# Kernel tuning notes

Measured on AMD Instinct MI355X. Metric: run time of the kernel, lower is better.

## Reference

```python
import jax, jax.numpy as jnp
import numpy as np
import math

EMB = 1024
HEADS = 16
VOCAB = 32000


def gelu_tanh(x):
    c = math.sqrt(2.0 / math.pi)
    return 0.5 * x * (1.0 + jnp.tanh(c * (x + 0.044715 * x * x * x)))


def layernorm(x, w, b, eps=1e-5):
    mean = jnp.mean(x, axis=-1, keepdims=True)
    var = jnp.var(x, axis=-1, keepdims=True)  # unbiased=False
    return w * ((x - mean) / jnp.sqrt(var + eps)) + b


def setup_inputs() -> dict:
    key = jax.random.key(0)
    ks = jax.random.split(key, 12)
    E, H, V = EMB, HEADS, VOCAB
    s = 1.0 / math.sqrt(E)
    return {
        "x": jax.random.normal(ks[0], (2, 2048, E), dtype=jnp.float32),
        "W_q": jax.random.normal(ks[1], (E, E), dtype=jnp.float32) * s,
        "W_k": jax.random.normal(ks[2], (E, E), dtype=jnp.float32) * s,
        "W_v": jax.random.normal(ks[3], (E, E), dtype=jnp.float32) * s,
        "ln1_w": jnp.ones((E,), jnp.float32),
        "ln1_b": jnp.zeros((E,), jnp.float32),
        "ln2_w": jnp.ones((E,), jnp.float32),
        "ln2_b": jnp.zeros((E,), jnp.float32),
        "ff_w1": jax.random.normal(ks[4], (E, 4 * E), dtype=jnp.float32) * s,
        "ff_b1": jnp.zeros((4 * E,), jnp.float32),
        "ff_w2": jax.random.normal(ks[5], (4 * E, E), dtype=jnp.float32) * (0.5 * s),
        "ff_b2": jnp.zeros((E,), jnp.float32),
        "proj_w": jax.random.normal(ks[6], (E, V), dtype=jnp.float32) * s,
        "proj_b": jnp.zeros((V,), jnp.float32),
    }


def attention(x, W_q, W_k, W_v):
    B, S, E = x.shape
    H = HEADS
    D = E // H
    q = (x @ W_q).reshape(B, S, H, D).transpose(0, 2, 1, 3)  # [B,H,S,D]
    k = (x @ W_k).reshape(B, S, H, D).transpose(0, 2, 1, 3)
    v = (x @ W_v).reshape(B, S, H, D).transpose(0, 2, 1, 3)
    scores = jnp.einsum("bhqd,bhkd->bhqk", q, k) / math.sqrt(D)
    causal = jnp.tril(jnp.ones((S, S), dtype=bool))
    scores = jnp.where(causal[None, None], scores, -jnp.inf)
    w = jax.nn.softmax(scores, axis=-1)
    ctx = jnp.einsum("bhqk,bhkd->bhqd", w, v)
    return ctx.transpose(0, 2, 1, 3).reshape(B, S, E)


def reference(x, W_q, W_k, W_v, ln1_w, ln1_b, ln2_w, ln2_b,
              ff_w1, ff_b1, ff_w2, ff_b2, proj_w, proj_b):
    # pre-LN attention block (dropout = identity, drop_rate=0)
    h = x + attention(layernorm(x, ln1_w, ln1_b), W_q, W_k, W_v)
    # pre-LN FFN block
    ff_in = layernorm(h, ln2_w, ln2_b)
    ff = gelu_tanh(ff_in @ ff_w1 + ff_b1) @ ff_w2 + ff_b2
    h = h + ff
    return h @ proj_w + proj_b
```

## Files before the change

### kernel.cpp

```cpp
#include <hip/hip_runtime.h>

using u16 = unsigned short;
typedef __attribute__((ext_vector_type(8))) short bf16x8;
typedef __attribute__((ext_vector_type(4))) float f32x4;

#define DEVI __device__ __forceinline__

DEVI float bf2f(u16 u){ union{ unsigned v; float f; } x; x.v = ((unsigned)u)<<16; return x.f; }
DEVI u16 f2bf(float f){ union{ float f; unsigned v; } x; x.f = f;
  unsigned r = x.v + 0x7FFFu + ((x.v>>16)&1u); return (u16)(r>>16); }

DEVI float gelu_f(float x){
  float y = 0.7978845608028654f*(x + 0.044715f*x*x*x);
  y = fminf(fmaxf(y, -30.f), 30.f);
  float e = __expf(2.f*y);
  return 0.5f*x*(1.f + (e-1.f)/(e+1.f));
}

DEVI void gload_lds16(const void* g, void* l){
  __builtin_amdgcn_global_load_lds((const __attribute__((address_space(1))) void*)g,
                                   (__attribute__((address_space(3))) void*)l, 16, 0, 0);
}

#define BARM asm volatile("s_barrier" ::: "memory")
#define LGKM0 asm volatile("s_waitcnt lgkmcnt(0)" ::: "memory")
#define VM8  asm volatile("s_waitcnt vmcnt(8)"  ::: "memory")
#define VM0  asm volatile("s_waitcnt vmcnt(0)"  ::: "memory")

__global__ __launch_bounds__(256) void wconv_kernel(const float* __restrict__ in,
                                                    u16* __restrict__ out, int R, int C){
  __shared__ u16 t[32][33];
  int c0 = blockIdx.x*32, r0 = blockIdx.y*32;
  int tc = threadIdx.x & 31, tr = threadIdx.x >> 5;
  #pragma unroll
  for (int i=0;i<4;i++){
    int r = tr + i*8;
    t[r][tc] = f2bf(in[(size_t)(r0+r)*C + (c0+tc)]);
  }
  __syncthreads();
  #pragma unroll
  for (int i=0;i<4;i++){
    int r = tr + i*8;
    out[(size_t)(c0+r)*R + (r0+tc)] = t[tc][r];
  }
}

DEVI void block_reduce2(float& s1, float& s2, int tid){
  #pragma unroll
  for (int off=1; off<64; off<<=1){ s1 += __shfl_xor(s1, off); s2 += __shfl_xor(s2, off); }
  __shared__ float red[8];
  int wid = tid>>6;
  if ((tid&63)==0){ red[wid*2]=s1; red[wid*2+1]=s2; }
  __syncthreads();
  s1 = red[0]+red[2]+red[4]+red[6];
  s2 = red[1]+red[3]+red[5]+red[7];
}

__global__ __launch_bounds__(256) void ln_kernel(const float* __restrict__ x,
    const float* __restrict__ w, const float* __restrict__ b, u16* __restrict__ out){
  int row = blockIdx.x, tid = threadIdx.x;
  float4 v = ((const float4*)(x + (size_t)row*1024))[tid];
  float s1 = v.x+v.y+v.z+v.w;
  float s2 = v.x*v.x+v.y*v.y+v.z*v.z+v.w*v.w;
  block_reduce2(s1,s2,tid);
  float mean = s1*(1.f/1024.f);
  float var  = s2*(1.f/1024.f) - mean*mean;
  float inv  = rsqrtf(var + 1e-5f);
  float4 wv = ((const float4*)w)[tid];
  float4 bv = ((const float4*)b)[tid];
  ushort4 o;
  o.x = f2bf(wv.x*((v.x-mean)*inv)+bv.x);
  o.y = f2bf(wv.y*((v.y-mean)*inv)+bv.y);
  o.z = f2bf(wv.z*((v.z-mean)*inv)+bv.z);
  o.w = f2bf(wv.w*((v.w-mean)*inv)+bv.w);
  ((ushort4*)(out + (size_t)row*1024))[tid] = o;
}

__global__ __launch_bounds__(256) void resln_kernel(const float* __restrict__ x,
    const u16* __restrict__ ctx, const float* __restrict__ w, const float* __restrict__ b,
    float* __restrict__ h, u16* __restrict__ hb){
  int row = blockIdx.x, tid = threadIdx.x;
  float4 xv = ((const float4*)(x + (size_t)row*1024))[tid];
  ushort4 cv = ((const ushort4*)(ctx + (size_t)row*1024))[tid];
  float4 hv;
  hv.x = xv.x + bf2f(cv.x); hv.y = xv.y + bf2f(cv.y);
  hv.z = xv.z + bf2f(cv.z); hv.w = xv.w + bf2f(cv.w);
  ((float4*)(h + (size_t)row*1024))[tid] = hv;
  float s1 = hv.x+hv.y+hv.z+hv.w;
  float s2 = hv.x*hv.x+hv.y*hv.y+hv.z*hv.z+hv.w*hv.w;
  block_reduce2(s1,s2,tid);
  float mean = s1*(1.f/1024.f);
  float var  = s2*(1.f/1024.f) - mean*mean;
  float inv  = rsqrtf(var + 1e-5f);
  float4 wv = ((const float4*)w)[tid];
  float4 bv = ((const float4*)b)[tid];
  ushort4 o;
  o.x = f2bf(wv.x*((hv.x-mean)*inv)+bv.x);
  o.y = f2bf(wv.y*((hv.y-mean)*inv)+bv.y);
  o.z = f2bf(wv.z*((hv.z-mean)*inv)+bv.z);
  o.w = f2bf(wv.w*((hv.w-mean)*inv)+bv.w);
  ((ushort4*)(hb + (size_t)row*1024))[tid] = o;
}

template<class EpiF>
DEVI void gemm8_core(const u16* __restrict__ A, const u16* __restrict__ Bt,
                     int K, int m0, int n0, EpiF epi){
  __shared__ __align__(16) u16 As[2][16384];
  __shared__ __align__(16) u16 Bs[2][16384];
  const int tid = threadIdx.x;
  const int wid = tid>>6, lane = tid&63;
  const int wr = wid>>2, wc = wid&3;
  const int g = lane>>4, l16 = lane&15;
  const int wq = wid&3;
  const int lr = lane>>3, ls = lane&7;

  f32x4 acc[8][4] = {};

  const u16* aSrc[2][2]; unsigned aDst[2][2];
  #pragma unroll
  for (int qm=0;qm<2;qm++)
    #pragma unroll
    for (int j=0;j<2;j++){
      int r = wr*128 + qm*64 + wq*16 + j*8 + lr;
      aSrc[qm][j] = A + (size_t)(m0 + r)*K + ((ls ^ (r&7))*8);
      aDst[qm][j] = (unsigned)(((wr*128 + qm*64)*8 + (wq*2+j)*64)*16);
    }
  const u16* bSrc[2][2]; unsigned bDst[2][2];
  #pragma unroll
  for (int qn=0;qn<2;qn++)
    #pragma unroll
    for (int j=0;j<2;j++){
      int r = wc*64 + qn*32 + wr*16 + j*8 + lr;
      bSrc[qn][j] = Bt + (size_t)(n0 + r)*K + ((ls ^ (r&7))*8);
      bDst[qn][j] = (unsigned)(((wc*64 + qn*32)*8 + (wr*2+j)*64)*16);
    }

  auto stageAll = [&](int buf, int kc){
    char* ab = (char*)&As[buf][0];
    char* bb = (char*)&Bs[buf][0];
    #pragma unroll
    for (int j=0;j<2;j++) gload_lds16(aSrc[0][j] + kc, ab + aDst[0][j]);
    #pragma unroll
    for (int j=0;j<2;j++) gload_lds16(bSrc[0][j] + kc, bb + bDst[0][j]);
    #pragma unroll
    for (int j=0;j<2;j++) gload_lds16(bSrc[1][j] + kc, bb + bDst[1][j]);
    #pragma unroll
    for (int j=0;j<2;j++) gload_lds16(aSrc[1][j] + kc, ab + aDst[1][j]);
  };
  auto ldA = [&](int buf, int qm, bf16x8 (&a)[4][2]){
    const char* base = (const char*)&As[buf][0];
    #pragma unroll
    for (int i=0;i<4;i++){
      int r = wr*128 + qm*64 + i*16 + l16;
      #pragma unroll
      for (int kk=0;kk<2;kk++)
        a[i][kk] = *(const bf16x8*)(base + r*128 + ((kk*64 + g*16) ^ ((l16&7)<<4)));
    }
  };
  auto ldB = [&](int buf, int qn, bf16x8 (&b)[2][2]){
    const char* base = (const char*)&Bs[buf][0];
    #pragma unroll
    for (int i=0;i<2;i++){
      int r = wc*64 + qn*32 + i*16 + l16;
      #pragma unroll
      for (int kk=0;kk<2;kk++)
        b[i][kk] = *(const bf16x8*)(base + r*128 + ((kk*64 + g*16) ^ ((l16&7)<<4)));
    }
  };
  auto mm = [&](int qm, int qn, bf16x8 (&a)[4][2], bf16x8 (&b)[2][2]){
    __builtin_amdgcn_s_setprio(1);
    #pragma unroll
    for (int i=0;i<4;i++)
      #pragma unroll
      for (int n=0;n<2;n++)
        #pragma unroll
        for (int kk=0;kk<2;kk++)
          acc[qm*4+i][qn*2+n] =
            __builtin_amdgcn_mfma_f32_16x16x32_bf16(a[i][kk], b[n][kk], acc[qm*4+i][qn*2+n], 0,0,0);
    __builtin_amdgcn_s_setprio(0);
  };

  const int NT = K>>6;
  stageAll(0, 0);
  stageAll(1, 64);

  bf16x8 a[4][2], b0[2][2], b1[2][2];
  int cur = 0;
  for (int t=0; t<NT; ++t){
    if (t < NT-1) { VM8; } else { VM0; }
    BARM;
    ldA(cur,0,a); ldB(cur,0,b0); ldB(cur,1,b1);
    mm(0,0,a,b0);
    mm(0,1,a,b1);
    ldA(cur,1,a);
    LGKM0; BARM;
    if (t+2 < NT) stageAll(cur, (t+2)<<6);
    mm(1,0,a,b0);
    mm(1,1,a,b1);
    cur ^= 1;
  }
  BARM;
  epi((char*)&As[0][0], (char*)&Bs[0][0], acc);
}

DEVI int xcd_swz(int id, int nwg){ return (id&7)*(nwg>>3) + (id>>3); }

__global__ __launch_bounds__(512,2) void proj8_kernel(const u16* __restrict__ hfb,
    const u16* __restrict__ pwt, const float* __restrict__ pb, float* __restrict__ out){
  const int xcd = blockIdx.x & 7, c = blockIdx.x >> 3;
  const int mt = 2*xcd + (c & 1);
  const int nt = c >> 1;
  const int m0 = mt*256, n0 = nt*256;
  gemm8_core(hfb, pwt, 1024, m0, n0,
    [&](char* sA, char* sB, f32x4 (&acc)[8][4]){
      const int tid = threadIdx.x;
      const int wid = tid>>6, lane = tid&63;
      const int wr = wid>>2, wc = wid&3;
      const int g = lane>>4, l16 = lane&15;
      float* ep = (float*)((wid<4 ? sA : sB) + (wid&3)*16384);
      float bb[4];
      #pragma unroll
      for (int nf=0;nf<4;nf++) bb[nf] = pb[n0 + wc*64 + nf*16 + l16];
      #pragma unroll
      for (int p=0;p<2;p++){
        #pragma unroll
        for (int mf4=0;mf4<4;mf4++){
          int mf = p*4 + mf4;
          #pragma unroll
          for (int nf=0;nf<4;nf++){
            #pragma unroll
            for (int r=0;r<4;r++)
              ep[(mf4*16 + g*4 + r)*64 + nf*16 + l16] = acc[mf][nf][r] + bb[nf];
          }
        }
        LGKM0;
        #pragma unroll
        for (int it=0;it<16;it++){
          int rl = it*4 + g;
          f32x4 v = *(const f32x4*)&ep[rl*64 + l16*4];
          int grow = m0 + wr*128 + p*64 + rl;
          __builtin_nontemporal_store(v,
            (f32x4*)&out[(size_t)grow*32000 + n0 + wc*64 + l16*4]);
        }
        LGKM0;
      }
    });
}

__global__ __launch_bounds__(512,2) void ffn1_8_kernel(const u16* __restrict__ hb,
    const u16* __restrict__ w1t, const float* __restrict__ b1, u16* __restrict__ gout){
  int swz = xcd_swz(blockIdx.x, gridDim.x);
  int mt = swz & 15, nt = swz >> 4;
  const int m0 = mt*256, n0 = nt*256;
  gemm8_core(hb, w1t, 1024, m0, n0,
    [&](char*, char*, f32x4 (&acc)[8][4]){
      const int tid = threadIdx.x;
      const int wid = tid>>6, lane = tid&63;
      const int wr = wid>>2, wc = wid&3;
      const int g = lane>>4, l16 = lane&15;
      #pragma unroll
      for (int mf=0;mf<8;mf++)
        #pragma unroll
        for (int nf=0;nf<4;nf++){
          int row = m0 + wr*128 + mf*16 + g*4;
          int col = n0 + wc*64 + nf*16 + l16;
          float bb = b1[col];
          #pragma unroll
          for (int r=0;r<4;r++)
            gout[(size_t)(row+r)*4096 + col] = f2bf(gelu_f(acc[mf][nf][r] + bb));
        }
    });
}

__global__ __launch_bounds__(512,2) void qkv8_kernel(const u16* __restrict__ xn,
    const u16* __restrict__ wqt, const u16* __restrict__ wkt, const u16* __restrict__ wvt,
    u16* __restrict__ qo, u16* __restrict__ ko, u16* __restrict__ vo){
  int swz = xcd_swz(blockIdx.x, gridDim.x);
  int mt = swz & 15, ntt = swz >> 4;
  int sel = ntt >> 2;
  const u16* Bt = (sel==0)?wqt:((sel==1)?wkt:wvt);
  u16* outp = (sel==0)?qo:((sel==1)?ko:vo);
  const int m0 = mt*256, n0 = (ntt&3)*256;
  gemm8_core(xn, Bt, 1024, m0, n0,
    [&](char*, char*, f32x4 (&acc)[8][4]){
      const int tid = threadIdx.x;
      const int wid = tid>>6, lane = tid&63;
      const int wr = wid>>2, wc = wid&3;
      const int g = lane>>4, l16 = lane&15;
      #pragma unroll
      for (int mf=0;mf<8;mf++)
        #pragma unroll
        for (int nf=0;nf<4;nf++){
          int row = m0 + wr*128 + mf*16 + g*4;
          int col = n0 + wc*64 + nf*16 + l16;
          #pragma unroll
          for (int r=0;r<4;r++)
            outp[(size_t)(row+r)*1024 + col] = f2bf(acc[mf][nf][r]);
        }
    });
}

template<int BM,int BN,int WM,int WN, class EpiF>
DEVI void gemm_core(const u16* __restrict__ A, const u16* __restrict__ Bt,
                    int K, int m0, int n0, EpiF epi){
  constexpr int WAVES_N = BN/WN;
  static_assert((BM/WM)*(BN/WN) == 4, "4 waves");
  constexpr int FM = WM/16, FN = WN/16;
  __shared__ u16 As[2][BM*32];
  __shared__ u16 Bs[2][BN*32];
  const int tid = threadIdx.x;
  const int wid = tid>>6, lane = tid&63;
  const int wr = wid / WAVES_N, wc = wid % WAVES_N;
  const int g = lane>>4, l16 = lane&15;
  f32x4 acc[FM][FN] = {};

  auto stage = [&](int buf, int t){
    #pragma unroll
    for (int j=0;j<BM/64;j++){
      int cbase = wid*BM + j*64;
      int c = cbase + lane;
      int r = c>>2, c4 = c&3;
      gload_lds16(A + (size_t)(m0+r)*K + t*32 + c4*8, &As[buf][cbase*8]);
    }
    #pragma unroll
    for (int j=0;j<BN/64;j++){
      int cbase = wid*BN + j*64;
      int c = cbase + lane;
      int r = c>>2, c4 = c&3;
      gload_lds16(Bt + (size_t)(n0+r)*K + t*32 + c4*8, &Bs[buf][cbase*8]);
    }
  };

  const int NT = K/32;
  stage(0,0);
  __syncthreads();
  for (int t=0;t<NT;t++){
    int cur = t&1;
    if (t+1 < NT) stage(cur^1, t+1);
    bf16x8 a[FM], b[FN];
    #pragma unroll
    for (int m=0;m<FM;m++) a[m] = *(const bf16x8*)&As[cur][(wr*WM + m*16 + l16)*32 + g*8];
    #pragma unroll
    for (int n=0;n<FN;n++) b[n] = *(const bf16x8*)&Bs[cur][(wc*WN + n*16 + l16)*32 + g*8];
    #pragma unroll
    for (int m=0;m<FM;m++)
      #pragma unroll
      for (int n=0;n<FN;n++)
        acc[m][n] = __builtin_amdgcn_mfma_f32_16x16x32_bf16(a[m], b[n], acc[m][n], 0,0,0);
    __syncthreads();
  }
  #pragma unroll
  for (int m=0;m<FM;m++)
    #pragma unroll
    for (int n=0;n<FN;n++){
      int row = m0 + wr*WM + m*16 + g*4;
      int col = n0 + wc*WN + n*16 + l16;
      epi(row, col, acc[m][n]);
    }
}

__global__ __launch_bounds__(256) void ffn2_kernel(const u16* __restrict__ gin,
    const u16* __restrict__ w2t, const float* __restrict__ b2,
    const float* __restrict__ h, u16* __restrict__ hfb){
  gemm_core<64,128,32,64>(gin, w2t, 4096, blockIdx.x*64, blockIdx.y*128,
    [&](int row,int col,f32x4 v){
      #pragma unroll
      for (int r=0;r<4;r++){
        float t = h[(size_t)(row+r)*1024 + col] + v[r] + b2[col];
        hfb[(size_t)(row+r)*1024 + col] = f2bf(t);
      }
    });
}

__global__ __launch_bounds__(256) void attn_kernel(const u16* __restrict__ q,
    const u16* __restrict__ k, const u16* __restrict__ v, u16* __restrict__ ctx){
  __shared__ u16 Qs[64*64], Ks[64*64], Vt[64*64];
  __shared__ u16 Ps[4][16*64];
  const int tid = threadIdx.x, lane = tid&63, wid = tid>>6;
  const int g = lane>>4, l16 = lane&15;
  const int b = blockIdx.x>>4, hh = blockIdx.x&15;
  const int qb = blockIdx.y;
  const size_t tokbase = (size_t)b*2048;
  const int hoff = hh*64;

  #pragma unroll
  for (int j=0;j<2;j++){
    int c = j*256 + tid;
    int r = c>>3, c8 = c&7;
    uint4 val = *(const uint4*)(q + (tokbase + qb*64 + r)*1024 + hoff + c8*8);
    *(uint4*)((char*)Qs + r*128 + ((c8*16) ^ ((r&7)<<4))) = val;
  }
  __syncthreads();
  bf16x8 qa[2];
  const int qrow_l = wid*16 + l16;
  #pragma unroll
  for (int kk=0;kk<2;kk++)
    qa[kk] = *(const bf16x8*)((const char*)Qs + qrow_l*128 + ((kk*64 + g*16) ^ ((qrow_l&7)<<4)));

  float m_r[4], l_r[4];
  f32x4 o_acc[4] = {};
  #pragma unroll
  for (int r=0;r<4;r++){ m_r[r] = -1e30f; l_r[r] = 0.f; }

  for (int kt=0; kt<=qb; kt++){
    __syncthreads();
    const int kv0 = kt*64;
    #pragma unroll
    for (int j=0;j<2;j++){
      int c = j*256 + tid;
      int r = c>>3, c8 = c&7;
      uint4 val = *(const uint4*)(k + (tokbase + kv0 + r)*1024 + hoff + c8*8);
      *(uint4*)((char*)Ks + r*128 + ((c8*16) ^ ((r&7)<<4))) = val;
    }
    #pragma unroll
    for (int j=0;j<2;j++){
      int c = j*256 + tid;
      int kv = c>>3, d8 = c&7;
      union{ uint4 u; u16 s[8]; } uu;
      uu.u = *(const uint4*)(v + (tokbase + kv0 + kv)*1024 + hoff + d8*8);
      #pragma unroll
      for (int e=0;e<8;e++){
        int d = d8*8+e;
        *(u16*)((char*)Vt + d*128 + ((kv*2) ^ ((d&7)<<4))) = uu.s[e];
      }
    }
    __syncthreads();

    f32x4 s[4] = {};
    #pragma unroll
    for (int c=0;c<4;c++){
      #pragma unroll
      for (int kk=0;kk<2;kk++){
        int krow = c*16 + l16;
        bf16x8 kb = *(const bf16x8*)((const char*)Ks + krow*128 + ((kk*64 + g*16) ^ ((krow&7)<<4)));
        s[c] = __builtin_amdgcn_mfma_f32_16x16x32_bf16(qa[kk], kb, s[c], 0,0,0);
      }
    }
    const int qrow0 = qb*64 + wid*16 + g*4;
    float sv[4][4];
    #pragma unroll
    for (int c=0;c<4;c++){
      #pragma unroll
      for (int r=0;r<4;r++){
        float xx = s[c][r] * 0.125f;
        if (kt==qb){
          int kvabs = kv0 + c*16 + l16;
          if (kvabs > qrow0 + r) xx = -1e30f;
        }
        sv[c][r] = xx;
      }
    }
    #pragma unroll
    for (int r=0;r<4;r++){
      float rm = fmaxf(fmaxf(sv[0][r],sv[1][r]),fmaxf(sv[2][r],sv[3][r]));
      #pragma unroll
      for (int off=1; off<16; off<<=1) rm = fmaxf(rm, __shfl_xor(rm, off));
      float mn  = fmaxf(m_r[r], rm);
      float fac = __expf(m_r[r] - mn);
      float rs = 0.f;
      const int prow = g*4 + r;
      #pragma unroll
      for (int c=0;c<4;c++){
        float p = __expf(sv[c][r] - mn);
        rs += p;
        *(u16*)((char*)&Ps[wid][0] + prow*128 + (((c*16+l16)*2) ^ ((prow&7)<<4))) = f2bf(p);
      }
      #pragma unroll
      for (int off=1; off<16; off<<=1) rs += __shfl_xor(rs, off);
      m_r[r] = mn;
      l_r[r] = l_r[r]*fac + rs;
      #pragma unroll
      for (int c=0;c<4;c++) o_acc[c][r] *= fac;
    }
    bf16x8 pa[2];
    #pragma unroll
    for (int kk=0;kk<2;kk++)
      pa[kk] = *(const bf16x8*)((const char*)&Ps[wid][0] + l16*128 + ((kk*64 + g*16) ^ ((l16&7)<<4)));
    #pragma unroll
    for (int c=0;c<4;c++){
      #pragma unroll
      for (int kk=0;kk<2;kk++){
        int vrow = c*16 + l16;
        bf16x8 vb = *(const bf16x8*)((const char*)Vt + vrow*128 + ((kk*64 + g*16) ^ ((vrow&7)<<4)));
        o_acc[c] = __builtin_amdgcn_mfma_f32_16x16x32_bf16(pa[kk], vb, o_acc[c], 0,0,0);
      }
    }
  }
  #pragma unroll
  for (int c=0;c<4;c++){
    #pragma unroll
    for (int r=0;r<4;r++){
      float o = o_acc[c][r] / l_r[r];
      size_t tok = tokbase + qb*64 + wid*16 + g*4 + r;
      ctx[tok*1024 + hoff + c*16 + l16] = f2bf(o);
    }
  }
}

extern "C" void kernel_launch(void* const* d_in, const int* in_sizes, int n_in,
                              void* d_out, int out_size, void* d_ws, size_t ws_size,
                              hipStream_t stream){
  (void)in_sizes; (void)n_in; (void)out_size; (void)ws_size;
  const float* x    = (const float*)d_in[0];
  const float* Wq   = (const float*)d_in[1];
  const float* Wk   = (const float*)d_in[2];
  const float* Wv   = (const float*)d_in[3];
  const float* ln1w = (const float*)d_in[4];
  const float* ln1b = (const float*)d_in[5];
  const float* ln2w = (const float*)d_in[6];
  const float* ln2b = (const float*)d_in[7];
  const float* fw1  = (const float*)d_in[8];
  const float* fb1  = (const float*)d_in[9];
  const float* fw2  = (const float*)d_in[10];
  const float* fb2  = (const float*)d_in[11];
  const float* pw   = (const float*)d_in[12];
  const float* pb   = (const float*)d_in[13];

  char* ob = (char*)d_out;
  u16* wqt = (u16*)(ob + 0);
  u16* wkt = (u16*)(ob + 2097152);
  u16* wvt = (u16*)(ob + 4194304);
  u16* w1t = (u16*)(ob + 6291456);
  u16* w2t = (u16*)(ob + 14680064);
  u16* xn  = (u16*)(ob + 23068672);
  u16* qbf = (u16*)(ob + 31457280);
  u16* kbf = (u16*)(ob + 39845888);
  u16* vbf = (u16*)(ob + 48234496);
  u16* ctx = (u16*)(ob + 56623104);
  float* h = (float*)(ob + 65011712);
  u16* hb  = (u16*)(ob + 81788928);
  u16* gbuf= (u16*)(ob + 90177536);

  char* wsb = (char*)d_ws;
  u16* pwt = (u16*)(wsb + 0);
  u16* hfb = (u16*)(wsb + 65536000);

  wconv_kernel<<<dim3(32,32)  ,256,0,stream>>>(Wq , wqt, 1024, 1024);
  wconv_kernel<<<dim3(32,32)  ,256,0,stream>>>(Wk , wkt, 1024, 1024);
  wconv_kernel<<<dim3(32,32)  ,256,0,stream>>>(Wv , wvt, 1024, 1024);
  wconv_kernel<<<dim3(128,32) ,256,0,stream>>>(fw1, w1t, 1024, 4096);
  wconv_kernel<<<dim3(32,128) ,256,0,stream>>>(fw2, w2t, 4096, 1024);
  wconv_kernel<<<dim3(1000,32),256,0,stream>>>(pw , pwt, 1024, 32000);

  ln_kernel    <<<4096,256,0,stream>>>(x, ln1w, ln1b, xn);
  qkv8_kernel  <<<192,512,0,stream>>>(xn, wqt, wkt, wvt, qbf, kbf, vbf);
  attn_kernel  <<<dim3(32,32),256,0,stream>>>(qbf, kbf, vbf, ctx);
  resln_kernel <<<4096,256,0,stream>>>(x, ctx, ln2w, ln2b, h, hb);
  ffn1_8_kernel<<<256,512,0,stream>>>(hb, w1t, fb1, gbuf);
  ffn2_kernel  <<<dim3(64,8) ,256,0,stream>>>(gbuf, w2t, fb2, h, hfb);
  proj8_kernel <<<2000,512,0,stream>>>(hfb, pwt, pb, (float*)d_out);
}
```

Before: 656.2 us.

## Use 128x128 pipelined GEMM core for FFN2 and double-buffer attention K/V tiles

Replaces the FFN2 kernel's simple 64x128 GEMM with a new 128x128 tile core. The core uses swizzled direct-to-LDS loads with two-stage prefetch, split MFMA phases with raised wave priority, and an XCD-aware tile mapping. It also double-buffers the K/V tiles in the attention kernel, prefetching the next tile into registers while the current one is being computed, which removes one barrier per iteration. The changes aim to hide global load latency and improve data reuse, at the cost of more LDS and register use and fewer blocks for FFN2.

```diff
diff --git a/kernel.cpp b/kernel.cpp
--- a/kernel.cpp
+++ b/kernel.cpp
@@ -203,6 +203,94 @@
   epi((char*)&As[0][0], (char*)&Bs[0][0], acc);
 }
 
+template<class EpiF>
+DEVI void gemm128_core(const u16* __restrict__ A, const u16* __restrict__ Bt,
+                       int K, int m0, int n0, EpiF epi){
+  __shared__ __align__(16) u16 As[2][8192];
+  __shared__ __align__(16) u16 Bs[2][8192];
+  const int tid = threadIdx.x;
+  const int wid = tid>>6, lane = tid&63;
+  const int wr = wid>>1, wc = wid&1;
+  const int g = lane>>4, l16 = lane&15;
+  const int lr = lane>>3, ls = lane&7;
+
+  f32x4 acc[4][4] = {};
+
+  const u16* aSrc[4]; unsigned aDst[4];
+  const u16* bSrc[4];
+  #pragma unroll
+  for (int j=0;j<4;j++){
+    int r = wid*32 + j*8 + lr;
+    aSrc[j] = A  + (size_t)(m0 + r)*K + ((ls ^ lr)*8);
+    bSrc[j] = Bt + (size_t)(n0 + r)*K + ((ls ^ lr)*8);
+    aDst[j] = (unsigned)((wid*32 + j*8)*128);
+  }
+
+  auto stageAll = [&](int buf, int kc){
+    char* ab = (char*)&As[buf][0];
+    char* bb = (char*)&Bs[buf][0];
+    #pragma unroll
+    for (int j=0;j<4;j++) gload_lds16(aSrc[j] + kc, ab + aDst[j]);
+    #pragma unroll
+    for (int j=0;j<4;j++) gload_lds16(bSrc[j] + kc, bb + aDst[j]);
+  };
+  auto ldA = [&](int buf, bf16x8 (&a)[4][2]){
+    const char* base = (const char*)&As[buf][0];
+    #pragma unroll
+    for (int i=0;i<4;i++){
+      int r = wr*64 + i*16 + l16;
+      #pragma unroll
+      for (int kk=0;kk<2;kk++)
+        a[i][kk] = *(const bf16x8*)(base + r*128 + ((kk*64 + g*16) ^ ((l16&7)<<4)));
+    }
+  };
+  auto ldB = [&](int buf, bf16x8 (&b)[4][2]){
+    const char* base = (const char*)&Bs[buf][0];
+    #pragma unroll
+    for (int i=0;i<4;i++){
+      int r = wc*64 + i*16 + l16;
+      #pragma unroll
+      for (int kk=0;kk<2;kk++)
+        b[i][kk] = *(const bf16x8*)(base + r*128 + ((kk*64 + g*16) ^ ((l16&7)<<4)));
+    }
+  };
+
+  const int NT = K>>6;
+  stageAll(0, 0);
+  stageAll(1, 64);
+
+  bf16x8 a[4][2], b[4][2];
+  int cur = 0;
+  for (int t=0; t<NT; ++t){
+    if (t < NT-1) { VM8; } else { VM0; }
+    BARM;
+    ldA(cur, a); ldB(cur, b);
+    __builtin_amdgcn_s_setprio(1);
+    #pragma unroll
+    for (int i=0;i<2;i++)
+      #pragma unroll
+      for (int n=0;n<4;n++)
+        #pragma unroll
+        for (int kk=0;kk<2;kk++)
+          acc[i][n] = __builtin_amdgcn_mfma_f32_16x16x32_bf16(a[i][kk], b[n][kk], acc[i][n], 0,0,0);
+    __builtin_amdgcn_s_setprio(0);
+    LGKM0; BARM;
+    if (t+2 < NT) stageAll(cur, (t+2)<<6);
+    __builtin_amdgcn_s_setprio(1);
+    #pragma unroll
+    for (int i=2;i<4;i++)
+      #pragma unroll
+      for (int n=0;n<4;n++)
+        #pragma unroll
+        for (int kk=0;kk<2;kk++)
+          acc[i][n] = __builtin_amdgcn_mfma_f32_16x16x32_bf16(a[i][kk], b[n][kk], acc[i][n], 0,0,0);
+    __builtin_amdgcn_s_setprio(0);
+    cur ^= 1;
+  }
+  BARM;
+  epi(acc);
+}
+
 DEVI int xcd_swz(int id, int nwg){ return (id&7)*(nwg>>3) + (id>>3); }
 
 __global__ __launch_bounds__(512,2) void proj8_kernel(const u16* __restrict__ hfb,
@@ -300,81 +388,38 @@
     });
 }
 
-template<int BM,int BN,int WM,int WN, class EpiF>
-DEVI void gemm_core(const u16* __restrict__ A, const u16* __restrict__ Bt,
-                    int K, int m0, int n0, EpiF epi){
-  constexpr int WAVES_N = BN/WN;
-  static_assert((BM/WM)*(BN/WN) == 4, "4 waves");
-  constexpr int FM = WM/16, FN = WN/16;
-  __shared__ u16 As[2][BM*32];
-  __shared__ u16 Bs[2][BN*32];
-  const int tid = threadIdx.x;
-  const int wid = tid>>6, lane = tid&63;
-  const int wr = wid / WAVES_N, wc = wid % WAVES_N;
-  const int g = lane>>4, l16 = lane&15;
-  f32x4 acc[FM][FN] = {};
-
-  auto stage = [&](int buf, int t){
-    #pragma unroll
-    for (int j=0;j<BM/64;j++){
-      int cbase = wid*BM + j*64;
-      int c = cbase + lane;
-      int r = c>>2, c4 = c&3;
-      gload_lds16(A + (size_t)(m0+r)*K + t*32 + c4*8, &As[buf][cbase*8]);
-    }
-    #pragma unroll
-    for (int j=0;j<BN/64;j++){
-      int cbase = wid*BN + j*64;
-      int c = cbase + lane;
-      int r = c>>2, c4 = c&3;
-      gload_lds16(Bt + (size_t)(n0+r)*K + t*32 + c4*8, &Bs[buf][cbase*8]);
-    }
-  };
-
-  const int NT = K/32;
-  stage(0,0);
-  __syncthreads();
-  for (int t=0;t<NT;t++){
-    int cur = t&1;
-    if (t+1 < NT) stage(cur^1, t+1);
-    bf16x8 a[FM], b[FN];
-    #pragma unroll
-    for (int m=0;m<FM;m++) a[m] = *(const bf16x8*)&As[cur][(wr*WM + m*16 + l16)*32 + g*8];
-    #pragma unroll
-    for (int n=0;n<FN;n++) b[n] = *(const bf16x8*)&Bs[cur][(wc*WN + n*16 + l16)*32 + g*8];
-    #pragma unroll
-    for (int m=0;m<FM;m++)
-      #pragma unroll
-      for (int n=0;n<FN;n++)
-        acc[m][n] = __builtin_amdgcn_mfma_f32_16x16x32_bf16(a[m], b[n], acc[m][n], 0,0,0);
-    __syncthreads();
-  }
-  #pragma unroll
-  for (int m=0;m<FM;m++)
-    #pragma unroll
-    for (int n=0;n<FN;n++){
-      int row = m0 + wr*WM + m*16 + g*4;
-      int col = n0 + wc*WN + n*16 + l16;
-      epi(row, col, acc[m][n]);
-    }
-}
-
-__global__ __launch_bounds__(256) void ffn2_kernel(const u16* __restrict__ gin,
+__global__ __launch_bounds__(256,2) void ffn2_kernel(const u16* __restrict__ gin,
     const u16* __restrict__ w2t, const float* __restrict__ b2,
     const float* __restrict__ h, u16* __restrict__ hfb){
-  gemm_core<64,128,32,64>(gin, w2t, 4096, blockIdx.x*64, blockIdx.y*128,
-    [&](int row,int col,f32x4 v){
-      #pragma unroll
-      for (int r=0;r<4;r++){
-        float t = h[(size_t)(row+r)*1024 + col] + v[r] + b2[col];
-        hfb[(size_t)(row+r)*1024 + col] = f2bf(t);
-      }
+  const int xcd = blockIdx.x & 7, c = blockIdx.x >> 3;
+  const int mt = 4*xcd + (c & 3);
+  const int nt = c >> 2;
+  const int m0 = mt*128, n0 = nt*128;
+  gemm128_core(gin, w2t, 4096, m0, n0,
+    [&](f32x4 (&acc)[4][4]){
+      const int tid = threadIdx.x;
+      const int wid = tid>>6, lane = tid&63;
+      const int wr = wid>>1, wc = wid&1;
+      const int g = lane>>4, l16 = lane&15;
+      #pragma unroll
+      for (int i=0;i<4;i++)
+        #pragma unroll
+        for (int nf=0;nf<4;nf++){
+          int row = m0 + wr*64 + i*16 + g*4;
+          int col = n0 + wc*64 + nf*16 + l16;
+          float bb = b2[col];
+          #pragma unroll
+          for (int r=0;r<4;r++)
+            hfb[(size_t)(row+r)*1024 + col] =
+              f2bf(h[(size_t)(row+r)*1024 + col] + acc[i][nf][r] + bb);
+        }
     });
 }
 
 __global__ __launch_bounds__(256) void attn_kernel(const u16* __restrict__ q,
     const u16* __restrict__ k, const u16* __restrict__ v, u16* __restrict__ ctx){
-  __shared__ u16 Qs[64*64], Ks[64*64], Vt[64*64];
+  __shared__ u16 Qs[64*64];
+  __shared__ u16 Ks[2][64*64], Vt[2][64*64];
   __shared__ u16 Ps[4][16*64];
   const int tid = threadIdx.x, lane = tid&63, wid = tid>>6;
   const int g = lane>>4, l16 = lane&15;
@@ -390,7 +435,28 @@
     uint4 val = *(const uint4*)(q + (tokbase + qb*64 + r)*1024 + hoff + c8*8);
     *(uint4*)((char*)Qs + r*128 + ((c8*16) ^ ((r&7)<<4))) = val;
   }
+  uint4 kreg[2], vreg[2];
+  #pragma unroll
+  for (int j=0;j<2;j++){
+    int c = j*256 + tid;
+    int r = c>>3, c8 = c&7;
+    kreg[j] = *(const uint4*)(k + (tokbase + r)*1024 + hoff + c8*8);
+    vreg[j] = *(const uint4*)(v + (tokbase + r)*1024 + hoff + c8*8);
+  }
+  #pragma unroll
+  for (int j=0;j<2;j++){
+    int c = j*256 + tid;
+    int r = c>>3, c8 = c&7;
+    *(uint4*)((char*)&Ks[0][0] + r*128 + ((c8*16) ^ ((r&7)<<4))) = kreg[j];
+    union{ uint4 u; u16 s[8]; } uu; uu.u = vreg[j];
+    #pragma unroll
+    for (int e=0;e<8;e++){
+      int d = c8*8 + e;
+      *(u16*)((char*)&Vt[0][0] + d*128 + ((r*2) ^ ((d&7)<<4))) = uu.s[e];
+    }
+  }
   __syncthreads();
+
   bf16x8 qa[2];
   const int qrow_l = wid*16 + l16;
   #pragma unroll
@@ -403,36 +469,25 @@
   for (int r=0;r<4;r++){ m_r[r] = -1e30f; l_r[r] = 0.f; }
 
   for (int kt=0; kt<=qb; kt++){
-    __syncthreads();
+    const int cur = kt&1, nxt = cur^1;
+    if (kt < qb){
+      const int kv0n = (kt+1)*64;
+      #pragma unroll
+      for (int j=0;j<2;j++){
+        int c = j*256 + tid;
+        int r = c>>3, c8 = c&7;
+        kreg[j] = *(const uint4*)(k + (tokbase + kv0n + r)*1024 + hoff + c8*8);
+        vreg[j] = *(const uint4*)(v + (tokbase + kv0n + r)*1024 + hoff + c8*8);
+      }
+    }
     const int kv0 = kt*64;
-    #pragma unroll
-    for (int j=0;j<2;j++){
-      int c = j*256 + tid;
-      int r = c>>3, c8 = c&7;
-      uint4 val = *(const uint4*)(k + (tokbase + kv0 + r)*1024 + hoff + c8*8);
-      *(uint4*)((char*)Ks + r*128 + ((c8*16) ^ ((r&7)<<4))) = val;
-    }
-    #pragma unroll
-    for (int j=0;j<2;j++){
-      int c = j*256 + tid;
-      int kv = c>>3, d8 = c&7;
-      union{ uint4 u; u16 s[8]; } uu;
-      uu.u = *(const uint4*)(v + (tokbase + kv0 + kv)*1024 + hoff + d8*8);
-      #pragma unroll
-      for (int e=0;e<8;e++){
-        int d = d8*8+e;
-        *(u16*)((char*)Vt + d*128 + ((kv*2) ^ ((d&7)<<4))) = uu.s[e];
-      }
-    }
-    __syncthreads();
-
     f32x4 s[4] = {};
     #pragma unroll
     for (int c=0;c<4;c++){
       #pragma unroll
       for (int kk=0;kk<2;kk++){
         int krow = c*16 + l16;
-        bf16x8 kb = *(const bf16x8*)((const char*)Ks + krow*128 + ((kk*64 + g*16) ^ ((krow&7)<<4)));
+        bf16x8 kb = *(const bf16x8*)((const char*)&Ks[cur][0] + krow*128 + ((kk*64 + g*16) ^ ((krow&7)<<4)));
         s[c] = __builtin_amdgcn_mfma_f32_16x16x32_bf16(qa[kk], kb, s[c], 0,0,0);
       }
     }
@@ -481,10 +536,25 @@
       #pragma unroll
       for (int kk=0;kk<2;kk++){
         int vrow = c*16 + l16;
-        bf16x8 vb = *(const bf16x8*)((const char*)Vt + vrow*128 + ((kk*64 + g*16) ^ ((vrow&7)<<4)));
+        bf16x8 vb = *(const bf16x8*)((const char*)&Vt[cur][0] + vrow*128 + ((kk*64 + g*16) ^ ((vrow&7)<<4)));
         o_acc[c] = __builtin_amdgcn_mfma_f32_16x16x32_bf16(pa[kk], vb, o_acc[c], 0,0,0);
       }
     }
+    if (kt < qb){
+      #pragma unroll
+      for (int j=0;j<2;j++){
+        int c = j*256 + tid;
+        int r = c>>3, c8 = c&7;
+        *(uint4*)((char*)&Ks[nxt][0] + r*128 + ((c8*16) ^ ((r&7)<<4))) = kreg[j];
+        union{ uint4 u; u16 s[8]; } uu; uu.u = vreg[j];
+        #pragma unroll
+        for (int e=0;e<8;e++){
+          int d = c8*8 + e;
+          *(u16*)((char*)&Vt[nxt][0] + d*128 + ((r*2) ^ ((d&7)<<4))) = uu.s[e];
+        }
+      }
+    }
+    __syncthreads();
   }
   #pragma unroll
   for (int c=0;c<4;c++){
@@ -547,6 +617,6 @@
   attn_kernel  <<<dim3(32,32),256,0,stream>>>(qbf, kbf, vbf, ctx);
   resln_kernel <<<4096,256,0,stream>>>(x, ctx, ln2w, ln2b, h, hb);
   ffn1_8_kernel<<<256,512,0,stream>>>(hb, w1t, fb1, gbuf);
-  ffn2_kernel  <<<dim3(64,8) ,256,0,stream>>>(gbuf, w2t, fb2, h, hfb);
+  ffn2_kernel  <<<256,256,0,stream>>>(gbuf, w2t, fb2, h, hfb);
   proj8_kernel <<<2000,512,0,stream>>>(hfb, pwt, pb, (float*)d_out);
 }
```

New measurement: 636.2 us. 3.0% less time.
